# Kernel optimization log

Measured on AMD Instinct MI355X. Metric: run time of the kernel, lower is better.

Reference implementation:

```python
import jax, jax.numpy as jnp
import numpy as np

DIM = 512
HEADS = 8
P = 4  # split_size
SCALE = (DIM // HEADS) ** -0.5  # scale uses full dim//heads as in source


def conv1x1(x, w):
    # x: [b,c,h,w], w: [out,in]
    return jnp.einsum('oc,bchw->bohw', w, x)


def to_windows(t, p1, p2, h):
    # 'b (h d) (x p1) (y p2) -> (b x y) h (p1 p2) d'
    b, c, X, Y = t.shape
    d = c // h
    nx, ny = X // p1, Y // p2
    t = t.reshape(b, h, d, nx, p1, ny, p2)
    t = t.transpose(0, 3, 5, 1, 4, 6, 2)  # b nx ny h p1 p2 d
    return t.reshape(b * nx * ny, h, p1 * p2, d)


def from_windows(t, b, nx, ny, h, p1, p2, d):
    # '(b x y) h (p1 p2) d -> b (h d) (x p1) (y p2)'
    t = t.reshape(b, nx, ny, h, p1, p2, d)
    t = t.transpose(0, 3, 6, 1, 4, 2, 5)  # b h d nx p1 ny p2
    return t.reshape(b, h * d, nx * p1, ny * p2)


def setup_inputs() -> dict:
    key = jax.random.key(0)
    ks = jax.random.split(key, 6)
    s = 0.02
    return {
        'fmap': jax.random.normal(ks[0], (8, DIM, 64, 64), jnp.float32),
        'w_qk': jax.random.normal(ks[1], (2 * DIM, DIM), jnp.float32) * s,
        'w_v': jax.random.normal(ks[2], (DIM, DIM), jnp.float32) * s,
        'w_v_vert': jax.random.normal(ks[3], (DIM // 2, DIM // 2), jnp.float32) * s,
        'w_v_horiz': jax.random.normal(ks[4], (DIM // 2, DIM // 2), jnp.float32) * s,
        'w_proj': jax.random.normal(ks[5], (DIM, DIM), jnp.float32) * s,
    }


def reference(fmap, w_qk, w_v, w_v_vert, w_v_horiz, w_proj):
    b, c, X, Y = fmap.shape
    h, half = HEADS, c // 2
    d = half // h  # per-window head dim

    qk = conv1x1(fmap, w_qk)
    q, k = jnp.split(qk, 2, axis=1)
    v = conv1x1(fmap, w_v)

    # horizontal branch: first half channels, windows (X, P)
    qh = to_windows(q[:, :half], X, P, h)
    kh = to_windows(k[:, :half], X, P, h)
    vh = to_windows(v[:, :half], X, P, h)
    lepe_h = vh  # source bug: to_v_horizontal output discarded, raw v used as LePE

    # vertical branch: second half channels, windows (P, Y)
    qv = to_windows(q[:, half:], P, Y, h)
    kv = to_windows(k[:, half:], P, Y, h)
    vv = to_windows(v[:, half:], P, Y, h)
    lepe_v = to_windows(conv1x1(v[:, half:], w_v_vert), P, Y, h)

    def attend(qw, kw, vw, lepe):
        attn = jax.nn.softmax((qw * SCALE) @ jnp.swapaxes(kw, -1, -2), axis=-1)
        return attn @ vw + lepe

    out_h = attend(qh, kh, vh, lepe_h)
    out_v = attend(qv, kv, vv, lepe_v)

    oh = from_windows(out_h, b, X // X, Y // P, h, X, P, d)
    ov = from_windows(out_v, b, X // P, Y // Y, h, P, Y, d)
    out = jnp.concatenate([oh, ov], axis=1)
    return fmap + conv1x1(out, w_proj)
```

## Files before the change

### kernel.cpp

```cpp
#include <hip/hip_runtime.h>
#include <hip/hip_bf16.h>

#define NPIX 4096
#define SCALE_L2E 0.18033688f

typedef unsigned short ushort_t;
typedef __attribute__((ext_vector_type(8))) short bf16x8;
typedef __attribute__((ext_vector_type(4))) float f32x4;
typedef __attribute__((ext_vector_type(8))) unsigned short us8;

__device__ __forceinline__ float bf2f(ushort_t u) {
  union { unsigned int i; float f; } v; v.i = ((unsigned int)u) << 16; return v.f;
}
__device__ __forceinline__ ushort_t f2bf(float f) {
  union { float f; unsigned int i; } v; v.f = f;
  unsigned int r = v.i + 0x7fffu + ((v.i >> 16) & 1u);
  return (ushort_t)(r >> 16);
}
__device__ __forceinline__ unsigned int cvtpk(float lo, float hi) {
  unsigned int r;
  asm volatile("v_cvt_pk_bf16_f32 %0, %1, %2" : "=v"(r) : "v"(lo), "v"(hi));
  return r;
}

__device__ __forceinline__ void gload16(const void* g, void* l) {
  __builtin_amdgcn_global_load_lds(
      (const __attribute__((address_space(1))) void*)g,
      (__attribute__((address_space(3))) void*)l, 16, 0, 0);
}

#define VMW(N) do { asm volatile("s_waitcnt vmcnt(" #N ")" ::: "memory"); \
                    __builtin_amdgcn_sched_barrier(0); } while (0)
#define LGKM0  do { asm volatile("s_waitcnt lgkmcnt(0)" ::: "memory");    \
                    __builtin_amdgcn_sched_barrier(0); } while (0)
#define BARR   __builtin_amdgcn_s_barrier()

__global__ __launch_bounds__(256) void cast_bf16(const float* __restrict__ s,
                                                 ushort_t* __restrict__ d, int n,
                                                 float scale) {
  int i = (blockIdx.x * 256 + threadIdx.x) * 4;
  if (i < n) {
    float4 v = *(const float4*)&s[i];
    ushort4 o = make_ushort4(f2bf(v.x * scale), f2bf(v.y * scale),
                             f2bf(v.z * scale), f2bf(v.w * scale));
    *(ushort4*)&d[i] = o;
  }
}

__global__ __launch_bounds__(256) void lepe_w(const float* __restrict__ wvv,
                                              const float* __restrict__ wv,
                                              ushort_t* __restrict__ out) {
  const int i = blockIdx.x, tid = threadIdx.x;
  float a0 = 0.f, a1 = 0.f;
  for (int c = 0; c < 256; ++c) {
    const float wc = wvv[i * 256 + c];
    a0 = fmaf(wc, wv[(size_t)(256 + c) * 512 + tid], a0);
    a1 = fmaf(wc, wv[(size_t)(256 + c) * 512 + 256 + tid], a1);
  }
  out[(size_t)i * 512 + tid] = f2bf(a0);
  out[(size_t)i * 512 + 256 + tid] = f2bf(a1);
}

__global__ __launch_bounds__(256) void transpose_cast(const float* __restrict__ fmap,
                                                      ushort_t* __restrict__ XT) {
  const int b = blockIdx.z, p0 = blockIdx.x * 64, c0 = blockIdx.y * 64;
  const int tid = threadIdx.x;
  __shared__ float t[64][65];
  const float* src = fmap + ((size_t)b * 512 + c0) * NPIX + p0;
  const int pr = tid & 63;
  #pragma unroll
  for (int i = 0; i < 16; ++i) {
    const int cr = i * 4 + (tid >> 6);
    t[cr][pr] = src[(size_t)cr * NPIX + pr];
  }
  __syncthreads();
  const int pw = tid >> 2, cwb = (tid & 3) * 16;
  us8 o0, o1;
  #pragma unroll
  for (int i = 0; i < 8; ++i) o0[i] = f2bf(t[cwb + i][pw]);
  #pragma unroll
  for (int i = 0; i < 8; ++i) o1[i] = f2bf(t[cwb + 8 + i][pw]);
  ushort_t* dst = XT + ((size_t)b * NPIX + p0 + pw) * 512 + c0 + cwb;
  *(us8*)&dst[0] = o0;
  *(us8*)&dst[8] = o1;
}

__global__ __launch_bounds__(512, 1) void gemm256(
    const ushort_t* __restrict__ A, const ushort_t* __restrict__ B,
    ushort_t* __restrict__ qkT, ushort_t* __restrict__ vbuf)
{
  const int b = blockIdx.z;
  const int p0 = blockIdx.x * 256;
  const int o0 = blockIdx.y * 256;
  const int tid = threadIdx.x;
  const int lane = tid & 63, w = tid >> 6;
  const int wm = w >> 2, wn = w & 3;
  const int g = lane >> 4, q16 = lane & 15;
  const int rl = lane >> 3, cc = lane & 7;
  const int cs = cc ^ rl;

  __shared__ __attribute__((aligned(16))) ushort_t lds[2 * 32768];

  const ushort_t* Bb = B + (size_t)b * NPIX * 512;

  f32x4 acc[8][4];
  #pragma unroll
  for (int m = 0; m < 8; ++m)
    #pragma unroll
    for (int n = 0; n < 4; ++n) acc[m][n] = (f32x4){0.f, 0.f, 0.f, 0.f};

  auto AHp = [&](int buf, int H) { return lds + buf * 32768 + H * 8192; };
  auto BHp = [&](int buf, int H) { return lds + buf * 32768 + 16384 + H * 8192; };

  auto stageA = [&](int buf, int H, int kb) {
    #pragma unroll
    for (int i = 0; i < 2; ++i) {
      const int row_g = o0 + i * 128 + H * 64 + w * 8 + rl;
      gload16(&A[(size_t)row_g * 512 + kb + cs * 8],
              AHp(buf, H) + (i * 64 + w * 8) * 64);
    }
  };
  auto stageB = [&](int buf, int H, int kb) {
    #pragma unroll
    for (int i = 0; i < 2; ++i) {
      const int stripe = i * 2 + (w >> 2);
      const int within = (w & 3) * 8 + rl;
      const int row_g = p0 + stripe * 64 + H * 32 + within;
      gload16(&Bb[(size_t)row_g * 512 + kb + cs * 8],
              BHp(buf, H) + (stripe * 32 + (w & 3) * 8) * 64);
    }
  };
  bf16x8 a[4][2], b01[2][2], b23[2][2];
  auto loadA = [&](int buf, int H) {
    #pragma unroll
    for (int mf = 0; mf < 4; ++mf)
      #pragma unroll
      for (int kk = 0; kk < 2; ++kk) {
        const int rr = wm * 64 + mf * 16 + q16;
        a[mf][kk] = *(const bf16x8*)&AHp(buf, H)[rr * 64 + ((kk * 4 + g) ^ (q16 & 7)) * 8];
      }
  };
  auto loadB = [&](bf16x8 bb[2][2], int buf, int H) {
    #pragma unroll
    for (int nf = 0; nf < 2; ++nf)
      #pragma unroll
      for (int kk = 0; kk < 2; ++kk) {
        const int rr = wn * 32 + nf * 16 + q16;
        bb[nf][kk] = *(const bf16x8*)&BHp(buf, H)[rr * 64 + ((kk * 4 + g) ^ (q16 & 7)) * 8];
      }
  };

#define MMA_Q(MH, NH, BB)                                                      \
  do {                                                                         \
    __builtin_amdgcn_s_setprio(1);                                             \
    _Pragma("unroll")                                                          \
    for (int mf = 0; mf < 4; ++mf)                                             \
      _Pragma("unroll")                                                        \
      for (int nf = 0; nf < 2; ++nf)                                           \
        _Pragma("unroll")                                                      \
        for (int kk = 0; kk < 2; ++kk)                                         \
          acc[(MH) * 4 + mf][(NH) * 2 + nf] =                                  \
              __builtin_amdgcn_mfma_f32_16x16x32_bf16(                         \
                  a[mf][kk], BB[nf][kk], acc[(MH) * 4 + mf][(NH) * 2 + nf],    \
                  0, 0, 0);                                                    \
    __builtin_amdgcn_s_setprio(0);                                             \
  } while (0)

  stageA(0, 0, 0); stageB(0, 0, 0); stageB(0, 1, 0); stageA(0, 1, 0);
  VMW(4);
  BARR;

  #pragma unroll 1
  for (int kt = 0; kt < 7; ++kt) {
    const int c = kt & 1, n = c ^ 1;
    const int kn = (kt + 1) * 64;
    loadA(c, 0); loadB(b01, c, 0);
    stageA(n, 0, kn);
    LGKM0;
    MMA_Q(0, 0, b01);
    VMW(4); BARR;
    loadB(b23, c, 1);
    stageB(n, 0, kn);
    LGKM0;
    MMA_Q(0, 1, b23);
    VMW(4); BARR;
    loadA(c, 1);
    stageB(n, 1, kn);
    LGKM0;
    MMA_Q(1, 1, b23);
    stageA(n, 1, kn);
    MMA_Q(1, 0, b01);
    VMW(4); BARR;
  }
  {
    loadA(1, 0); loadB(b01, 1, 0);
    LGKM0;
    MMA_Q(0, 0, b01);
    VMW(2); BARR;
    loadB(b23, 1, 1);
    LGKM0;
    MMA_Q(0, 1, b23);
    VMW(0); BARR;
    loadA(1, 1);
    LGKM0;
    MMA_Q(1, 1, b23);
    MMA_Q(1, 0, b01);
  }

  if (o0 < 1024) {
    ushort_t* CT = qkT + (size_t)b * NPIX * 1024;
    #pragma unroll
    for (int mf = 0; mf < 8; ++mf)
      #pragma unroll
      for (int nf = 0; nf < 4; ++nf) {
        const int pix = p0 + wn * 64 + nf * 16 + q16;
        const int chb = o0 + wm * 128 + mf * 16 + g * 4;
        ushort4 s4 = make_ushort4(f2bf(acc[mf][nf][0]), f2bf(acc[mf][nf][1]),
                                  f2bf(acc[mf][nf][2]), f2bf(acc[mf][nf][3]));
        *(ushort4*)&CT[(size_t)pix * 1024 + chb] = s4;
      }
  } else {
    ushort_t* C = vbuf + (size_t)b * 768 * NPIX;
    #pragma unroll
    for (int mf = 0; mf < 8; ++mf)
      #pragma unroll
      for (int nf = 0; nf < 4; ++nf) {
        const int col = p0 + wn * 64 + nf * 16 + q16;
        #pragma unroll
        for (int j = 0; j < 4; ++j) {
          const int row = o0 - 1024 + wm * 128 + mf * 16 + g * 4 + j;
          C[(size_t)row * NPIX + col] = f2bf(acc[mf][nf][j]);
        }
      }
  }
#undef MMA_Q
}

__global__ __launch_bounds__(256) void gemm_proj(
    const ushort_t* __restrict__ A, const ushort_t* __restrict__ B,
    float* __restrict__ Cout, const float* __restrict__ Res)
{
  const int b = blockIdx.z;
  const int p0 = blockIdx.x * 128;
  const int o0 = blockIdx.y * 128;
  const int tid = threadIdx.x;
  const int lane = tid & 63, w = tid >> 6;
  const int wrow = (w >> 1) * 64, wcol = (w & 1) * 64;

  __shared__ __attribute__((aligned(16))) short As[128 * 32];
  __shared__ __attribute__((aligned(16))) short Bs[128 * 32];

  const ushort_t* Bb = B + (size_t)b * NPIX * 512;

  f32x4 acc[4][4];
  #pragma unroll
  for (int m = 0; m < 4; ++m)
    #pragma unroll
    for (int n = 0; n < 4; ++n) acc[m][n] = (f32x4){0.f, 0.f, 0.f, 0.f};

  const int cl = lane & 3;

  for (int kt = 0; kt < 16; ++kt) {
    const int kb = kt * 32;
    #pragma unroll
    for (int i = 0; i < 2; ++i) {
      const int r = w * 32 + i * 16 + (lane >> 2);
      const int cs = cl ^ ((r >> 1) & 3);
      gload16(&A[(size_t)(o0 + r) * 512 + kb + cs * 8], &As[(w * 32 + i * 16) * 32]);
      gload16(&Bb[(size_t)(p0 + r) * 512 + kb + cs * 8], &Bs[(w * 32 + i * 16) * 32]);
    }
    __syncthreads();
    bf16x8 af[4], bfr[4];
    #pragma unroll
    for (int m = 0; m < 4; ++m) {
      const int row = wrow + m * 16 + (lane & 15);
      const int c = (lane >> 4) ^ ((row >> 1) & 3);
      af[m] = *(const bf16x8*)&As[row * 32 + c * 8];
    }
    #pragma unroll
    for (int n = 0; n < 4; ++n) {
      const int row = wcol + n * 16 + (lane & 15);
      const int c = (lane >> 4) ^ ((row >> 1) & 3);
      bfr[n] = *(const bf16x8*)&Bs[row * 32 + c * 8];
    }
    #pragma unroll
    for (int m = 0; m < 4; ++m)
      #pragma unroll
      for (int n = 0; n < 4; ++n)
        acc[m][n] = __builtin_amdgcn_mfma_f32_16x16x32_bf16(af[m], bfr[n], acc[m][n], 0, 0, 0);
    __syncthreads();
  }

  const int fr = lane & 15, fq = lane >> 4;
  float* C = Cout + (size_t)b * 512 * NPIX;
  const float* R = Res + (size_t)b * 512 * NPIX;
  #pragma unroll
  for (int m = 0; m < 4; ++m)
    #pragma unroll
    for (int n = 0; n < 4; ++n) {
      const int col = p0 + wcol + n * 16 + fr;
      #pragma unroll
      for (int j = 0; j < 4; ++j) {
        const int row = o0 + wrow + m * 16 + fq * 4 + j;
        const size_t idx = (size_t)row * NPIX + col;
        C[idx] = acc[m][n][j] + R[idx];
      }
    }
}

__global__ __launch_bounds__(256) void attn_mfma(const ushort_t* __restrict__ qkT,
                                                 const ushort_t* __restrict__ vbuf,
                                                 ushort_t* __restrict__ attT) {
  const int hh = blockIdx.x, wi = blockIdx.y, vert = blockIdx.z;
  const int b = wi >> 4, iw = wi & 15;
  const int tid = threadIdx.x;
  const int lane = tid & 63, w = tid >> 6;
  const int g = lane >> 4, q16 = lane & 15;
  const int qbase = w * 64;

  __shared__ __attribute__((aligned(16))) ushort_t K_lds[256 * 32];
  __shared__ __attribute__((aligned(16))) ushort_t VT_lds[32 * 256];
  __shared__ __attribute__((aligned(16))) ushort_t P_lds[4][64 * 40];

  const ushort_t* QKb = qkT + (size_t)b * NPIX * 1024;

  #pragma unroll
  for (int it = 0; it < 4; ++it) {
    const int j = w * 64 + it * 16 + (lane >> 2);
    const int cs = (lane & 3) ^ ((j >> 1) & 3);
    const int pj = vert ? iw * 256 + j : (j >> 2) * 64 + iw * 4 + (j & 3);
    gload16(&QKb[(size_t)pj * 1024 + 512 + hh * 32 + cs * 8],
            &K_lds[(w * 64 + it * 16) * 32]);
  }
  const ushort_t* Vg = vbuf + ((size_t)b * 768 + vert * 256 + hh * 32) * (size_t)NPIX;
  #pragma unroll
  for (int it = 0; it < 8; ++it) {
    const int d = it * 4 + w;
    const int jg = lane;
    const int pb = vert ? iw * 256 + jg * 4 : jg * 64 + iw * 4;
    const ushort4 v4 = *(const ushort4*)&Vg[(size_t)d * NPIX + pb];
    *(ushort4*)&VT_lds[d * 256 + (((jg >> 1) ^ d) << 3) + ((jg & 1) << 2)] = v4;
  }
  bf16x8 qf[4];
  #pragma unroll
  for (int qt = 0; qt < 4; ++qt) {
    const int q = qbase + qt * 16 + q16;
    const int qp = vert ? iw * 256 + q : (q >> 2) * 64 + iw * 4 + (q & 3);
    qf[qt] = *(const bf16x8*)&QKb[(size_t)qp * 1024 + hh * 32 + g * 8];
  }
  __syncthreads();

  float l[4] = {0.f, 0.f, 0.f, 0.f};
  f32x4 o[4][2];
  #pragma unroll
  for (int qt = 0; qt < 4; ++qt) {
    o[qt][0] = (f32x4){0.f, 0.f, 0.f, 0.f};
    o[qt][1] = (f32x4){0.f, 0.f, 0.f, 0.f};
  }

  const f32x4 zero4 = (f32x4){0.f, 0.f, 0.f, 0.f};
  const int kc = g ^ ((q16 >> 1) & 3);

  for (int jc = 0; jc < 8; ++jc) {
    bf16x8 kf0 = *(const bf16x8*)&K_lds[(jc * 32 + q16) * 32 + kc * 8];
    bf16x8 kf1 = *(const bf16x8*)&K_lds[(jc * 32 + 16 + q16) * 32 + kc * 8];
    f32x4 st[2][4];
    #pragma unroll
    for (int qt = 0; qt < 4; ++qt) {
      st[0][qt] = __builtin_amdgcn_mfma_f32_16x16x32_bf16(kf0, qf[qt], zero4, 0, 0, 0);
      st[1][qt] = __builtin_amdgcn_mfma_f32_16x16x32_bf16(kf1, qf[qt], zero4, 0, 0, 0);
    }
    #pragma unroll
    for (int qt = 0; qt < 4; ++qt) {
      const float p00 = exp2f(st[0][qt][0]), p01 = exp2f(st[0][qt][1]);
      const float p02 = exp2f(st[0][qt][2]), p03 = exp2f(st[0][qt][3]);
      const float p10 = exp2f(st[1][qt][0]), p11 = exp2f(st[1][qt][1]);
      const float p12 = exp2f(st[1][qt][2]), p13 = exp2f(st[1][qt][3]);
      float rs = ((p00 + p01) + (p02 + p03)) + ((p10 + p11) + (p12 + p13));
      rs += __shfl_xor(rs, 16);
      rs += __shfl_xor(rs, 32);
      l[qt] += rs;
      uint2 pk0, pk1;
      pk0.x = cvtpk(p00, p01); pk0.y = cvtpk(p02, p03);
      pk1.x = cvtpk(p10, p11); pk1.y = cvtpk(p12, p13);
      *(uint2*)&P_lds[w][(qt * 16 + q16) * 40 + g * 4]      = pk0;
      *(uint2*)&P_lds[w][(qt * 16 + q16) * 40 + 16 + g * 4] = pk1;
    }
    const int vc0 = (jc * 4 + g) ^ q16;
    const int vc1 = (jc * 4 + g) ^ (16 + q16);
    bf16x8 vf0 = *(const bf16x8*)&VT_lds[q16 * 256 + vc0 * 8];
    bf16x8 vf1 = *(const bf16x8*)&VT_lds[(16 + q16) * 256 + vc1 * 8];
    #pragma unroll
    for (int qt = 0; qt < 4; ++qt) {
      bf16x8 pf = *(const bf16x8*)&P_lds[w][(qt * 16 + q16) * 40 + g * 8];
      o[qt][0] = __builtin_amdgcn_mfma_f32_16x16x32_bf16(pf, vf0, o[qt][0], 0, 0, 0);
      o[qt][1] = __builtin_amdgcn_mfma_f32_16x16x32_bf16(pf, vf1, o[qt][1], 0, 0, 0);
    }
  }

  const int ch = vert * 256 + hh * 32;
  const ushort_t* Lg = vbuf + ((size_t)b * 768 + 512 + hh * 32) * (size_t)NPIX;
  #pragma unroll
  for (int qt = 0; qt < 4; ++qt) {
    const float linv = 1.f / l[qt];
    float li[4];
    #pragma unroll
    for (int jj = 0; jj < 4; ++jj) li[jj] = __shfl(linv, g * 4 + jj);
    #pragma unroll
    for (int dt = 0; dt < 2; ++dt) {
      const int d = dt * 16 + q16;
      #pragma unroll
      for (int jj = 0; jj < 4; ++jj) {
        const int q = qbase + qt * 16 + g * 4 + jj;
        float lep;
        if (vert) lep = bf2f(Lg[(size_t)d * NPIX + iw * 256 + q]);
        else      lep = bf2f(VT_lds[d * 256 + (((q >> 3) ^ d) << 3) + (q & 7)]);
        const int pix = vert ? iw * 256 + q : (q >> 2) * 64 + iw * 4 + (q & 3);
        attT[((size_t)b * NPIX + pix) * 512 + ch + d] = f2bf(o[qt][dt][jj] * li[jj] + lep);
      }
    }
  }
}

extern "C" void kernel_launch(void* const* d_in, const int* in_sizes, int n_in,
                              void* d_out, int out_size, void* d_ws, size_t ws_size,
                              hipStream_t stream) {
  const float* fmap     = (const float*)d_in[0];
  const float* w_qk     = (const float*)d_in[1];
  const float* w_v      = (const float*)d_in[2];
  const float* w_v_vert = (const float*)d_in[3];
  const float* w_proj   = (const float*)d_in[5];
  float* out = (float*)d_out;

  ushort_t* XT   = (ushort_t*)d_ws;
  ushort_t* qkT  = XT + (size_t)8 * NPIX * 512;
  ushort_t* vbuf = qkT + (size_t)8 * NPIX * 1024;
  ushort_t* attT = vbuf + (size_t)8 * 768 * NPIX;
  ushort_t* WQKV = attT + (size_t)8 * NPIX * 512;
  ushort_t* WPb  = WQKV + (size_t)1792 * 512;

  dim3 blk(256);
  cast_bf16<<<256, blk, 0, stream>>>(w_qk, WQKV, 512 * 512, SCALE_L2E);
  cast_bf16<<<256, blk, 0, stream>>>(w_qk + (size_t)512 * 512,
                                     WQKV + (size_t)512 * 512, 512 * 512, 1.0f);
  cast_bf16<<<256, blk, 0, stream>>>(w_v, WQKV + (size_t)1024 * 512, 512 * 512, 1.0f);
  cast_bf16<<<256, blk, 0, stream>>>(w_proj, WPb, 512 * 512, 1.0f);
  lepe_w<<<256, blk, 0, stream>>>(w_v_vert, w_v, WQKV + (size_t)1536 * 512);
  transpose_cast<<<dim3(64, 8, 8), blk, 0, stream>>>(fmap, XT);
  gemm256<<<dim3(16, 7, 8), dim3(512), 0, stream>>>(WQKV, XT, qkT, vbuf);
  attn_mfma<<<dim3(8, 128, 2), blk, 0, stream>>>(qkT, vbuf, attT);
  gemm_proj<<<dim3(32, 4, 8), blk, 0, stream>>>(WPb, attT, out, fmap);
}
```

Measured before the change: 237.0 us.

## Reuse 256-tile pipelined GEMM for output projection and restage loads earlier

Removes the simple 128x128 projection GEMM and runs the output projection through the 256x256 double-buffered gemm256 kernel, with a mode flag selecting an fp32 residual-add epilogue. The main loop's prefetch schedule also changes: all four next-tile stage loads are issued in the first two phases instead of being spread across three, with matching wait counts. The goal is better data reuse and MFMA pipelining for the projection, and earlier overlap of global loads. In exchange the projection grid shrinks to 256 blocks of 512 threads, which may underfill the GPU, and the extra in-flight loads raise register and LDS pressure.

Result: no change. 234.8 us (-0.9%).

```diff
diff --git a/kernel.cpp b/kernel.cpp
--- a/kernel.cpp
+++ b/kernel.cpp
@@ -87,7 +87,8 @@
 
 __global__ __launch_bounds__(512, 1) void gemm256(
     const ushort_t* __restrict__ A, const ushort_t* __restrict__ B,
-    ushort_t* __restrict__ qkT, ushort_t* __restrict__ vbuf)
+    ushort_t* __restrict__ qkT, ushort_t* __restrict__ vbuf,
+    float* __restrict__ outF, const float* __restrict__ Res, int mode)
 {
   const int b = blockIdx.z;
   const int p0 = blockIdx.x * 256;
@@ -166,7 +167,8 @@
     __builtin_amdgcn_s_setprio(0);                                             \
   } while (0)
 
-  stageA(0, 0, 0); stageB(0, 0, 0); stageB(0, 1, 0); stageA(0, 1, 0);
+  stageA(0, 0, 0); stageB(0, 0, 0);
+  stageB(0, 1, 0); stageA(0, 1, 0);
   VMW(4);
   BARR;
 
@@ -175,20 +177,18 @@
     const int c = kt & 1, n = c ^ 1;
     const int kn = (kt + 1) * 64;
     loadA(c, 0); loadB(b01, c, 0);
-    stageA(n, 0, kn);
+    stageA(n, 0, kn); stageB(n, 0, kn);
     LGKM0;
     MMA_Q(0, 0, b01);
-    VMW(4); BARR;
+    VMW(6); BARR;
     loadB(b23, c, 1);
-    stageB(n, 0, kn);
+    stageB(n, 1, kn); stageA(n, 1, kn);
     LGKM0;
     MMA_Q(0, 1, b23);
-    VMW(4); BARR;
+    VMW(8); BARR;
     loadA(c, 1);
-    stageB(n, 1, kn);
     LGKM0;
     MMA_Q(1, 1, b23);
-    stageA(n, 1, kn);
     MMA_Q(1, 0, b01);
     VMW(4); BARR;
   }
@@ -207,20 +207,36 @@
     MMA_Q(1, 0, b01);
   }
 
-  if (o0 < 1024) {
-    ushort_t* CT = qkT + (size_t)b * NPIX * 1024;
-    #pragma unroll
-    for (int mf = 0; mf < 8; ++mf)
-      #pragma unroll
-      for (int nf = 0; nf < 4; ++nf) {
-        const int pix = p0 + wn * 64 + nf * 16 + q16;
-        const int chb = o0 + wm * 128 + mf * 16 + g * 4;
-        ushort4 s4 = make_ushort4(f2bf(acc[mf][nf][0]), f2bf(acc[mf][nf][1]),
-                                  f2bf(acc[mf][nf][2]), f2bf(acc[mf][nf][3]));
-        *(ushort4*)&CT[(size_t)pix * 1024 + chb] = s4;
-      }
+  if (mode == 0) {
+    if (o0 < 1024) {
+      ushort_t* CT = qkT + (size_t)b * NPIX * 1024;
+      #pragma unroll
+      for (int mf = 0; mf < 8; ++mf)
+        #pragma unroll
+        for (int nf = 0; nf < 4; ++nf) {
+          const int pix = p0 + wn * 64 + nf * 16 + q16;
+          const int chb = o0 + wm * 128 + mf * 16 + g * 4;
+          ushort4 s4 = make_ushort4(f2bf(acc[mf][nf][0]), f2bf(acc[mf][nf][1]),
+                                    f2bf(acc[mf][nf][2]), f2bf(acc[mf][nf][3]));
+          *(ushort4*)&CT[(size_t)pix * 1024 + chb] = s4;
+        }
+    } else {
+      ushort_t* C = vbuf + (size_t)b * 768 * NPIX;
+      #pragma unroll
+      for (int mf = 0; mf < 8; ++mf)
+        #pragma unroll
+        for (int nf = 0; nf < 4; ++nf) {
+          const int col = p0 + wn * 64 + nf * 16 + q16;
+          #pragma unroll
+          for (int j = 0; j < 4; ++j) {
+            const int row = o0 - 1024 + wm * 128 + mf * 16 + g * 4 + j;
+            C[(size_t)row * NPIX + col] = f2bf(acc[mf][nf][j]);
+          }
+        }
+    }
   } else {
-    ushort_t* C = vbuf + (size_t)b * 768 * NPIX;
+    float* C = outF + (size_t)b * 512 * NPIX;
+    const float* R = Res + (size_t)b * 512 * NPIX;
     #pragma unroll
     for (int mf = 0; mf < 8; ++mf)
       #pragma unroll
@@ -228,84 +244,13 @@
         const int col = p0 + wn * 64 + nf * 16 + q16;
         #pragma unroll
         for (int j = 0; j < 4; ++j) {
-          const int row = o0 - 1024 + wm * 128 + mf * 16 + g * 4 + j;
-          C[(size_t)row * NPIX + col] = f2bf(acc[mf][nf][j]);
+          const int row = o0 + wm * 128 + mf * 16 + g * 4 + j;
+          const size_t idx = (size_t)row * NPIX + col;
+          C[idx] = acc[mf][nf][j] + R[idx];
         }
       }
   }
 #undef MMA_Q
-}
-
-__global__ __launch_bounds__(256) void gemm_proj(
-    const ushort_t* __restrict__ A, const ushort_t* __restrict__ B,
-    float* __restrict__ Cout, const float* __restrict__ Res)
-{
-  const int b = blockIdx.z;
-  const int p0 = blockIdx.x * 128;
-  const int o0 = blockIdx.y * 128;
-  const int tid = threadIdx.x;
-  const int lane = tid & 63, w = tid >> 6;
-  const int wrow = (w >> 1) * 64, wcol = (w & 1) * 64;
-
-  __shared__ __attribute__((aligned(16))) short As[128 * 32];
-  __shared__ __attribute__((aligned(16))) short Bs[128 * 32];
-
-  const ushort_t* Bb = B + (size_t)b * NPIX * 512;
-
-  f32x4 acc[4][4];
-  #pragma unroll
-  for (int m = 0; m < 4; ++m)
-    #pragma unroll
-    for (int n = 0; n < 4; ++n) acc[m][n] = (f32x4){0.f, 0.f, 0.f, 0.f};
-
-  const int cl = lane & 3;
-
-  for (int kt = 0; kt < 16; ++kt) {
-    const int kb = kt * 32;
-    #pragma unroll
-    for (int i = 0; i < 2; ++i) {
-      const int r = w * 32 + i * 16 + (lane >> 2);
-      const int cs = cl ^ ((r >> 1) & 3);
-      gload16(&A[(size_t)(o0 + r) * 512 + kb + cs * 8], &As[(w * 32 + i * 16) * 32]);
-      gload16(&Bb[(size_t)(p0 + r) * 512 + kb + cs * 8], &Bs[(w * 32 + i * 16) * 32]);
-    }
-    __syncthreads();
-    bf16x8 af[4], bfr[4];
-    #pragma unroll
-    for (int m = 0; m < 4; ++m) {
-      const int row = wrow + m * 16 + (lane & 15);
-      const int c = (lane >> 4) ^ ((row >> 1) & 3);
-      af[m] = *(const bf16x8*)&As[row * 32 + c * 8];
-    }
-    #pragma unroll
-    for (int n = 0; n < 4; ++n) {
-      const int row = wcol + n * 16 + (lane & 15);
-      const int c = (lane >> 4) ^ ((row >> 1) & 3);
-      bfr[n] = *(const bf16x8*)&Bs[row * 32 + c * 8];
-    }
-    #pragma unroll
-    for (int m = 0; m < 4; ++m)
-      #pragma unroll
-      for (int n = 0; n < 4; ++n)
-        acc[m][n] = __builtin_amdgcn_mfma_f32_16x16x32_bf16(af[m], bfr[n], acc[m][n], 0, 0, 0);
-    __syncthreads();
-  }
-
-  const int fr = lane & 15, fq = lane >> 4;
-  float* C = Cout + (size_t)b * 512 * NPIX;
-  const float* R = Res + (size_t)b * 512 * NPIX;
-  #pragma unroll
-  for (int m = 0; m < 4; ++m)
-    #pragma unroll
-    for (int n = 0; n < 4; ++n) {
-      const int col = p0 + wcol + n * 16 + fr;
-      #pragma unroll
-      for (int j = 0; j < 4; ++j) {
-        const int row = o0 + wrow + m * 16 + fq * 4 + j;
-        const size_t idx = (size_t)row * NPIX + col;
-        C[idx] = acc[m][n][j] + R[idx];
-      }
-    }
 }
 
 __global__ __launch_bounds__(256) void attn_mfma(const ushort_t* __restrict__ qkT,
@@ -447,7 +392,9 @@
   cast_bf16<<<256, blk, 0, stream>>>(w_proj, WPb, 512 * 512, 1.0f);
   lepe_w<<<256, blk, 0, stream>>>(w_v_vert, w_v, WQKV + (size_t)1536 * 512);
   transpose_cast<<<dim3(64, 8, 8), blk, 0, stream>>>(fmap, XT);
-  gemm256<<<dim3(16, 7, 8), dim3(512), 0, stream>>>(WQKV, XT, qkT, vbuf);
+  gemm256<<<dim3(16, 7, 8), dim3(512), 0, stream>>>(
+      WQKV, XT, qkT, vbuf, nullptr, nullptr, 0);
   attn_mfma<<<dim3(8, 128, 2), blk, 0, stream>>>(qkT, vbuf, attT);
-  gemm_proj<<<dim3(32, 4, 8), blk, 0, stream>>>(WPb, attT, out, fmap);
-}
+  gemm256<<<dim3(16, 2, 8), dim3(512), 0, stream>>>(
+      WPb, attT, nullptr, nullptr, out, fmap, 1);
+}
```
